# Optimization experiments

Hardware: AMD Instinct MI355X
Metric: run time of the kernel (lower is better)

## Reference

```python
import jax, jax.numpy as jnp
import numpy as np

FEATURE_DIM = 256
NUM_COEDGES = 200000


def setup_inputs() -> dict:
    key = jax.random.key(0)
    ks = jax.random.split(key, 13)
    d = FEATURE_DIM
    n = NUM_COEDGES
    scale = 1.0 / np.sqrt(d)
    inp = {
        "features": jax.random.normal(ks[0], (n, d), dtype=jnp.float32),
        "next_indices": jax.random.randint(ks[1], (n,), 0, n),
        "prev_indices": jax.random.randint(ks[2], (n,), 0, n),
        "mate_indices": jax.random.randint(ks[3], (n,), 0, n),
        # Linear params (torch Linear: y = x @ W.T + b); store as [d, d] for x @ W
        "W_self": jax.random.uniform(ks[4], (d, d), jnp.float32, -scale, scale),
        "b_self": jax.random.uniform(ks[5], (d,), jnp.float32, -scale, scale),
        "W_next": jax.random.uniform(ks[6], (d, d), jnp.float32, -scale, scale),
        "b_next": jax.random.uniform(ks[7], (d,), jnp.float32, -scale, scale),
        "W_prev": jax.random.uniform(ks[8], (d, d), jnp.float32, -scale, scale),
        "b_prev": jax.random.uniform(ks[9], (d,), jnp.float32, -scale, scale),
        "W_mate": jax.random.uniform(ks[10], (d, d), jnp.float32, -scale, scale),
        "b_mate": jax.random.uniform(ks[11], (d,), jnp.float32, -scale, scale),
    }
    return inp


def reference(features, next_indices, prev_indices, mate_indices,
              W_self, b_self, W_next, b_next, W_prev, b_prev, W_mate, b_mate):
    h = features  # [n, d]
    h_self = h @ W_self + b_self
    h_next = h[next_indices] @ W_next + b_next
    h_prev = h[prev_indices] @ W_prev + b_prev
    h_mate = h[mate_indices] @ W_mate + b_mate
    return jax.nn.relu(h_self + h_next + h_prev + h_mate)
```

## Files before the change

### kernel.cpp

```cpp
#include <hip/hip_runtime.h>
#include <stdint.h>


#define D 256
#define BM 64

typedef __bf16 bf16x8 __attribute__((ext_vector_type(8)));
typedef float f32x4 __attribute__((ext_vector_type(4)));

static __device__ __forceinline__ uint16_t f32_to_bf16_rne(uint32_t u) {
    return (uint16_t)((u + 0x7FFFu + ((u >> 16) & 1u)) >> 16);
}

__global__ void k_conv(const float* __restrict__ f, uint16_t* __restrict__ o, long total) {
    long base = (long)blockIdx.x * 2048;
    int t = threadIdx.x;
#pragma unroll
    for (int pass = 0; pass < 2; pass++) {
        long i = base + pass * 1024 + (long)t * 4;
        if (i + 4 > total) return;
        uint32_t v[4];
        *(uint4*)v = *(const uint4*)(f + i);
        union { uint16_t u16[4]; uint2 v2; } r;
#pragma unroll
        for (int j = 0; j < 4; j++) r.u16[j] = f32_to_bf16_rne(v[j]);
        *(uint2*)(o + i) = r.v2;
    }
}

__global__ void k_pack(const float* __restrict__ Ws, const float* __restrict__ Wn,
                       const float* __restrict__ Wp, const float* __restrict__ Wm,
                       uint16_t* __restrict__ Bp) {
    int b = blockIdx.x;
    int l = threadIdx.x;
    int ksg = b >> 4, nt = b & 15;
    int ph = ksg >> 3;
    const float* W = (ph == 0) ? Ws : (ph == 1) ? Wn : (ph == 2) ? Wp : Wm;
    int kl = (ksg & 7) * 32 + (l >> 4) * 8;
    int n  = nt * 16 + (l & 15);
    uint16_t* dst = Bp + ((size_t)b * 64 + l) * 8;
#pragma unroll
    for (int j = 0; j < 8; j++) {
        uint32_t u = __builtin_bit_cast(uint32_t, W[(size_t)(kl + j) * D + n]);
        dst[j] = f32_to_bf16_rne(u);
    }
}

__global__ void k_bias(const float* __restrict__ b0, const float* __restrict__ b1,
                       const float* __restrict__ b2, const float* __restrict__ b3,
                       float* __restrict__ btot) {
    int t = threadIdx.x;
    if (t < D) btot[t] = b0[t] + b1[t] + b2[t] + b3[t];
}

typedef __attribute__((address_space(1))) uint32_t gu32;
typedef __attribute__((address_space(3))) uint32_t lu32;

__global__ __launch_bounds__(256, 2) void k_gemm(
    const uint16_t* __restrict__ fb,
    const int* __restrict__ ni, const int* __restrict__ pi, const int* __restrict__ mi,
    const uint16_t* __restrict__ Bp, const float* __restrict__ btot,
    float* __restrict__ out, int nrows)
{
    __shared__ uint16_t As[2][BM * D];
    const int t  = threadIdx.x;
    const int w  = t >> 6;
    const int l  = t & 63;
    const int ml = l & 15;
    const int q  = l >> 4;
    const int m0 = blockIdx.x * BM;

    f32x4 acc[4][4] = {};

    const int rpar = w * 16 + (l >> 5);
    const int cs   = l & 31;

    uint32_t off0[8], off1[8], off2[8], off3[8];
#pragma unroll
    for (int e = 0; e < 8; e++) {
        int r = rpar + e * 2;
        int rowg = m0 + r; if (rowg >= nrows) rowg = nrows - 1;
        uint32_t co = (uint32_t)((cs ^ (r & 7)) * 16);
        off0[e] = (uint32_t)rowg * (D * 2) + co;
        off1[e] = (uint32_t)ni[rowg] * (D * 2) + co;
        off2[e] = (uint32_t)pi[rowg] * (D * 2) + co;
        off3[e] = (uint32_t)mi[rowg] * (D * 2) + co;
    }

#define STAGE(OFFA, BUF) do { \
        uint16_t* _s = &As[BUF][(w * 16) * D]; \
        _Pragma("unroll") \
        for (int e = 0; e < 8; e++) { \
            const char* _g = (const char*)fb + (OFFA)[e]; \
            __builtin_amdgcn_global_load_lds((const gu32*)_g, (lu32*)(_s + e * 2 * D), 16, 0, 0); \
        } \
    } while (0)

#define KSTEP(BUF, BB, KS) do { \
        bf16x8 bfr[4]; \
        _Pragma("unroll") \
        for (int j = 0; j < 4; j++) bfr[j] = *(const bf16x8*)((BB) + ((KS) * 16 + j) * 512); \
        bf16x8 afr[4]; \
        _Pragma("unroll") \
        for (int mt = 0; mt < 4; mt++) { \
            int r = mt * 16 + ml; \
            int ch = ((KS) * 4 + q) ^ (r & 7); \
            afr[mt] = *(const bf16x8*)&As[BUF][r * D + ch * 8]; \
        } \
        _Pragma("unroll") \
        for (int mt = 0; mt < 4; mt++) \
            _Pragma("unroll") \
            for (int j = 0; j < 4; j++) \
                acc[mt][j] = __builtin_amdgcn_mfma_f32_16x16x32_bf16(afr[mt], bfr[j], acc[mt][j], 0, 0, 0); \
    } while (0)

#define KSTEP_PRE(BUF, BPRE, KS) do { \
        bf16x8 afr[4]; \
        _Pragma("unroll") \
        for (int mt = 0; mt < 4; mt++) { \
            int r = mt * 16 + ml; \
            int ch = ((KS) * 4 + q) ^ (r & 7); \
            afr[mt] = *(const bf16x8*)&As[BUF][r * D + ch * 8]; \
        } \
        _Pragma("unroll") \
        for (int mt = 0; mt < 4; mt++) \
            _Pragma("unroll") \
            for (int j = 0; j < 4; j++) \
                acc[mt][j] = __builtin_amdgcn_mfma_f32_16x16x32_bf16(afr[mt], (BPRE)[j], acc[mt][j], 0, 0, 0); \
    } while (0)

#define WAITBAR() do { \
        asm volatile("s_waitcnt vmcnt(0)" ::: "memory"); \
        __builtin_amdgcn_s_barrier(); \
        __builtin_amdgcn_sched_barrier(0); \
    } while (0)

#define PHASE(P, BUF, OFFNEXT, LAST) do { \
        WAITBAR(); \
        const uint16_t* bb = Bp + (((size_t)(P) * 128 + w * 4) * 64 + l) * 8; \
        KSTEP(BUF, bb, 0); KSTEP(BUF, bb, 1); KSTEP(BUF, bb, 2); \
        KSTEP(BUF, bb, 3); KSTEP(BUF, bb, 4); KSTEP(BUF, bb, 5); \
        bf16x8 b6[4], b7[4]; \
        _Pragma("unroll") \
        for (int j = 0; j < 4; j++) { \
            b6[j] = *(const bf16x8*)(bb + (6 * 16 + j) * 512); \
            b7[j] = *(const bf16x8*)(bb + (7 * 16 + j) * 512); \
        } \
        if (!(LAST)) { \
            __builtin_amdgcn_sched_barrier(0); \
            STAGE(OFFNEXT, (BUF) ^ 1); \
            __builtin_amdgcn_sched_barrier(0); \
        } \
        KSTEP_PRE(BUF, b6, 6); \
        KSTEP_PRE(BUF, b7, 7); \
    } while (0)

    STAGE(off0, 0);
    PHASE(0, 0, off1, 0);
    PHASE(1, 1, off2, 0);
    PHASE(2, 0, off3, 0);
    PHASE(3, 1, off0, 1);

#undef PHASE
#undef WAITBAR
#undef KSTEP_PRE
#undef KSTEP
#undef STAGE

#pragma unroll
    for (int j = 0; j < 4; j++) {
        int n = (w * 4 + j) * 16 + ml;
        float bv = btot[n];
#pragma unroll
        for (int mt = 0; mt < 4; mt++) {
#pragma unroll
            for (int rg = 0; rg < 4; rg++) {
                int row = m0 + mt * 16 + q * 4 + rg;
                if (row < nrows) {
                    float v = acc[mt][j][rg] + bv;
                    out[(size_t)row * D + n] = v > 0.f ? v : 0.f;
                }
            }
        }
    }
}

__global__ void k_naive(const float* __restrict__ f,
                        const int* __restrict__ ni, const int* __restrict__ pi,
                        const int* __restrict__ mi,
                        const float* __restrict__ Ws, const float* __restrict__ bs,
                        const float* __restrict__ Wn, const float* __restrict__ bn,
                        const float* __restrict__ Wp, const float* __restrict__ bp,
                        const float* __restrict__ Wm, const float* __restrict__ bm,
                        float* __restrict__ out) {
    int row = blockIdx.x, n = threadIdx.x;
    const float* f0 = f + (size_t)row * D;
    const float* f1 = f + (size_t)ni[row] * D;
    const float* f2 = f + (size_t)pi[row] * D;
    const float* f3 = f + (size_t)mi[row] * D;
    float s = bs[n] + bn[n] + bp[n] + bm[n];
    for (int k = 0; k < D; k++)
        s += f0[k] * Ws[k * D + n] + f1[k] * Wn[k * D + n] +
             f2[k] * Wp[k * D + n] + f3[k] * Wm[k * D + n];
    out[(size_t)row * D + n] = s > 0.f ? s : 0.f;
}

extern "C" void kernel_launch(void* const* d_in, const int* in_sizes, int n_in,
                              void* d_out, int out_size, void* d_ws, size_t ws_size,
                              hipStream_t stream) {
    const float* feat = (const float*)d_in[0];
    const int*   ni   = (const int*)d_in[1];
    const int*   pi   = (const int*)d_in[2];
    const int*   mi   = (const int*)d_in[3];
    const float* Ws   = (const float*)d_in[4];
    const float* bs   = (const float*)d_in[5];
    const float* Wn   = (const float*)d_in[6];
    const float* bn   = (const float*)d_in[7];
    const float* Wp   = (const float*)d_in[8];
    const float* bp   = (const float*)d_in[9];
    const float* Wm   = (const float*)d_in[10];
    const float* bm   = (const float*)d_in[11];
    float* out = (float*)d_out;

    int nrows = in_sizes[1];
    size_t feat_elems = (size_t)nrows * D;
    size_t fb_bytes   = feat_elems * 2;
    size_t bp_off     = fb_bytes;
    size_t bias_off   = bp_off + (size_t)1024 * D * 2;
    size_t need       = bias_off + (size_t)D * 4;

    if (ws_size < need) {
        k_naive<<<nrows, D, 0, stream>>>(feat, ni, pi, mi, Ws, bs, Wn, bn, Wp, bp, Wm, bm, out);
        return;
    }

    uint16_t* fbuf = (uint16_t*)d_ws;
    uint16_t* Bpk  = (uint16_t*)((char*)d_ws + bp_off);
    float*    btot = (float*)((char*)d_ws + bias_off);

    long total = (long)feat_elems;
    int cblocks = (int)((total + 2047) / 2048);
    k_conv<<<cblocks, 256, 0, stream>>>(feat, fbuf, total);
    k_pack<<<512, 64, 0, stream>>>(Ws, Wn, Wp, Wm, Bpk);
    k_bias<<<1, 256, 0, stream>>>(bs, bn, bp, bm, btot);
    k_gemm<<<(nrows + BM - 1) / BM, 256, 0, stream>>>(fbuf, ni, pi, mi, Bpk, btot, out, nrows);
}
```

Baseline: 537.6 us.

## Use 128-row tiles with 8 waves and register-staged single LDS buffer

The GEMM tile grows from 64 to 128 rows with 512 threads arranged as 2x4 waves, so each packed weight fragment loaded from global memory is reused across twice as many rows. The double-buffered LDS with async global_load_lds is replaced by register staging: the next phase's gathered rows go into registers during compute and are written to a single LDS buffer after a barrier. The bias-sum kernel is folded into the weight-pack kernel as an extra block, removing one launch. In exchange there is extra register pressure and a second barrier per phase, and the LDS write is no longer overlapped with compute.

After: 575.0 us. 7.0% more time.

```diff
diff --git a/kernel.cpp b/kernel.cpp
--- a/kernel.cpp
+++ b/kernel.cpp
@@ -3,7 +3,7 @@
 
 
 #define D 256
-#define BM 64
+#define BM 128
 
 typedef __bf16 bf16x8 __attribute__((ext_vector_type(8)));
 typedef float f32x4 __attribute__((ext_vector_type(4)));
@@ -30,9 +30,19 @@
 
 __global__ void k_pack(const float* __restrict__ Ws, const float* __restrict__ Wn,
                        const float* __restrict__ Wp, const float* __restrict__ Wm,
-                       uint16_t* __restrict__ Bp) {
+                       const float* __restrict__ bs, const float* __restrict__ bn,
+                       const float* __restrict__ bp, const float* __restrict__ bm,
+                       uint16_t* __restrict__ Bp, float* __restrict__ btot) {
     int b = blockIdx.x;
     int l = threadIdx.x;
+    if (b == 512) {
+#pragma unroll
+        for (int k = 0; k < 4; k++) {
+            int n = l + k * 64;
+            btot[n] = bs[n] + bn[n] + bp[n] + bm[n];
+        }
+        return;
+    }
     int ksg = b >> 4, nt = b & 15;
     int ph = ksg >> 3;
     const float* W = (ph == 0) ? Ws : (ph == 1) ? Wn : (ph == 2) ? Wp : Wm;
@@ -46,28 +56,20 @@
     }
 }
 
-__global__ void k_bias(const float* __restrict__ b0, const float* __restrict__ b1,
-                       const float* __restrict__ b2, const float* __restrict__ b3,
-                       float* __restrict__ btot) {
-    int t = threadIdx.x;
-    if (t < D) btot[t] = b0[t] + b1[t] + b2[t] + b3[t];
-}
-
-typedef __attribute__((address_space(1))) uint32_t gu32;
-typedef __attribute__((address_space(3))) uint32_t lu32;
-
-__global__ __launch_bounds__(256, 2) void k_gemm(
+__global__ __launch_bounds__(512, 2) void k_gemm(
     const uint16_t* __restrict__ fb,
     const int* __restrict__ ni, const int* __restrict__ pi, const int* __restrict__ mi,
     const uint16_t* __restrict__ Bp, const float* __restrict__ btot,
     float* __restrict__ out, int nrows)
 {
-    __shared__ uint16_t As[2][BM * D];
+    __shared__ uint16_t As[BM * D];
     const int t  = threadIdx.x;
     const int w  = t >> 6;
     const int l  = t & 63;
     const int ml = l & 15;
     const int q  = l >> 4;
+    const int wr = w >> 2;
+    const int wc = w & 3;
     const int m0 = blockIdx.x * BM;
 
     f32x4 acc[4][4] = {};
@@ -75,107 +77,99 @@
     const int rpar = w * 16 + (l >> 5);
     const int cs   = l & 31;
 
-    uint32_t off0[8], off1[8], off2[8], off3[8];
+    uint32_t off0[8], off1[8], off2[8], off3[8], loff[8];
 #pragma unroll
     for (int e = 0; e < 8; e++) {
         int r = rpar + e * 2;
         int rowg = m0 + r; if (rowg >= nrows) rowg = nrows - 1;
-        uint32_t co = (uint32_t)((cs ^ (r & 7)) * 16);
+        uint32_t co = (uint32_t)(cs * 16);
         off0[e] = (uint32_t)rowg * (D * 2) + co;
         off1[e] = (uint32_t)ni[rowg] * (D * 2) + co;
         off2[e] = (uint32_t)pi[rowg] * (D * 2) + co;
         off3[e] = (uint32_t)mi[rowg] * (D * 2) + co;
-    }
-
-#define STAGE(OFFA, BUF) do { \
-        uint16_t* _s = &As[BUF][(w * 16) * D]; \
-        _Pragma("unroll") \
-        for (int e = 0; e < 8; e++) { \
-            const char* _g = (const char*)fb + (OFFA)[e]; \
-            __builtin_amdgcn_global_load_lds((const gu32*)_g, (lu32*)(_s + e * 2 * D), 16, 0, 0); \
-        } \
-    } while (0)
-
-#define KSTEP(BUF, BB, KS) do { \
-        bf16x8 bfr[4]; \
-        _Pragma("unroll") \
-        for (int j = 0; j < 4; j++) bfr[j] = *(const bf16x8*)((BB) + ((KS) * 16 + j) * 512); \
-        bf16x8 afr[4]; \
+        loff[e] = (uint32_t)r * (D * 2) + (uint32_t)((cs ^ (r & 7)) * 16);
+    }
+
+    uint4 st[8];
+
+#define STAGE_LOAD(OFFA) do { \
+        _Pragma("unroll") \
+        for (int e = 0; e < 8; e++) \
+            st[e] = *(const uint4*)((const char*)fb + (OFFA)[e]); \
+    } while (0)
+
+#define STAGE_WRITE() do { \
+        _Pragma("unroll") \
+        for (int e = 0; e < 8; e++) \
+            *(uint4*)((char*)As + loff[e]) = st[e]; \
+    } while (0)
+
+#define LOADB(DST, KS) do { \
+        _Pragma("unroll") \
+        for (int j = 0; j < 4; j++) \
+            (DST)[j] = *(const bf16x8*)(bb + ((KS) * 16 + j) * 512); \
+    } while (0)
+
+#define MM(BREG, KS) do { \
         _Pragma("unroll") \
         for (int mt = 0; mt < 4; mt++) { \
-            int r = mt * 16 + ml; \
-            int ch = ((KS) * 4 + q) ^ (r & 7); \
-            afr[mt] = *(const bf16x8*)&As[BUF][r * D + ch * 8]; \
-        } \
-        _Pragma("unroll") \
-        for (int mt = 0; mt < 4; mt++) \
+            int r  = wr * 64 + mt * 16 + ml; \
+            int ch = ((KS) * 4 + q) ^ (r & 7);             \
+            bf16x8 afr = *(const bf16x8*)&As[r * D + ch * 8]; \
             _Pragma("unroll") \
             for (int j = 0; j < 4; j++) \
-                acc[mt][j] = __builtin_amdgcn_mfma_f32_16x16x32_bf16(afr[mt], bfr[j], acc[mt][j], 0, 0, 0); \
-    } while (0)
-
-#define KSTEP_PRE(BUF, BPRE, KS) do { \
-        bf16x8 afr[4]; \
-        _Pragma("unroll") \
-        for (int mt = 0; mt < 4; mt++) { \
-            int r = mt * 16 + ml; \
-            int ch = ((KS) * 4 + q) ^ (r & 7); \
-            afr[mt] = *(const bf16x8*)&As[BUF][r * D + ch * 8]; \
+                acc[mt][j] = __builtin_amdgcn_mfma_f32_16x16x32_bf16( \
+                    afr, (BREG)[j], acc[mt][j], 0, 0, 0); \
         } \
-        _Pragma("unroll") \
-        for (int mt = 0; mt < 4; mt++) \
-            _Pragma("unroll") \
-            for (int j = 0; j < 4; j++) \
-                acc[mt][j] = __builtin_amdgcn_mfma_f32_16x16x32_bf16(afr[mt], (BPRE)[j], acc[mt][j], 0, 0, 0); \
-    } while (0)
-
-#define WAITBAR() do { \
-        asm volatile("s_waitcnt vmcnt(0)" ::: "memory"); \
+    } while (0)
+
+#define PHASE(P, OFFNEXT, LAST) do { \
         __builtin_amdgcn_s_barrier(); \
         __builtin_amdgcn_sched_barrier(0); \
-    } while (0)
-
-#define PHASE(P, BUF, OFFNEXT, LAST) do { \
-        WAITBAR(); \
-        const uint16_t* bb = Bp + (((size_t)(P) * 128 + w * 4) * 64 + l) * 8; \
-        KSTEP(BUF, bb, 0); KSTEP(BUF, bb, 1); KSTEP(BUF, bb, 2); \
-        KSTEP(BUF, bb, 3); KSTEP(BUF, bb, 4); KSTEP(BUF, bb, 5); \
-        bf16x8 b6[4], b7[4]; \
-        _Pragma("unroll") \
-        for (int j = 0; j < 4; j++) { \
-            b6[j] = *(const bf16x8*)(bb + (6 * 16 + j) * 512); \
-            b7[j] = *(const bf16x8*)(bb + (7 * 16 + j) * 512); \
-        } \
+        STAGE_WRITE(); \
+        asm volatile("s_waitcnt lgkmcnt(0)" ::: "memory"); \
+        __builtin_amdgcn_s_barrier(); \
+        __builtin_amdgcn_sched_barrier(0); \
+        const uint16_t* bb = Bp + (((size_t)(P) * 128 + wc * 4) * 64 + l) * 8; \
+        bf16x8 Ba[4], Bb[4]; \
+        LOADB(Ba, 0); \
+        LOADB(Bb, 1); MM(Ba, 0); \
+        LOADB(Ba, 2); MM(Bb, 1); \
+        LOADB(Bb, 3); MM(Ba, 2); \
+        LOADB(Ba, 4); MM(Bb, 3); \
+        LOADB(Bb, 5); MM(Ba, 4); \
+        LOADB(Ba, 6); MM(Bb, 5); \
+        LOADB(Bb, 7); \
         if (!(LAST)) { \
             __builtin_amdgcn_sched_barrier(0); \
-            STAGE(OFFNEXT, (BUF) ^ 1); \
+            STAGE_LOAD(OFFNEXT); \
             __builtin_amdgcn_sched_barrier(0); \
         } \
-        KSTEP_PRE(BUF, b6, 6); \
-        KSTEP_PRE(BUF, b7, 7); \
-    } while (0)
-
-    STAGE(off0, 0);
-    PHASE(0, 0, off1, 0);
-    PHASE(1, 1, off2, 0);
-    PHASE(2, 0, off3, 0);
-    PHASE(3, 1, off0, 1);
+        MM(Ba, 6); \
+        MM(Bb, 7); \
+    } while (0)
+
+    STAGE_LOAD(off0);
+    PHASE(0, off1, 0);
+    PHASE(1, off2, 0);
+    PHASE(2, off3, 0);
+    PHASE(3, off0, 1);
 
 #undef PHASE
-#undef WAITBAR
-#undef KSTEP_PRE
-#undef KSTEP
-#undef STAGE
+#undef MM
+#undef LOADB
+#undef STAGE_WRITE
+#undef STAGE_LOAD
 
 #pragma unroll
     for (int j = 0; j < 4; j++) {
-        int n = (w * 4 + j) * 16 + ml;
+        int n = (wc * 4 + j) * 16 + ml;
         float bv = btot[n];
 #pragma unroll
         for (int mt = 0; mt < 4; mt++) {
 #pragma unroll
             for (int rg = 0; rg < 4; rg++) {
-                int row = m0 + mt * 16 + q * 4 + rg;
+                int row = m0 + wr * 64 + mt * 16 + q * 4 + rg;
                 if (row < nrows) {
                     float v = acc[mt][j][rg] + bv;
                     out[(size_t)row * D + n] = v > 0.f ? v : 0.f;
@@ -241,7 +235,6 @@
     long total = (long)feat_elems;
     int cblocks = (int)((total + 2047) / 2048);
     k_conv<<<cblocks, 256, 0, stream>>>(feat, fbuf, total);
-    k_pack<<<512, 64, 0, stream>>>(Ws, Wn, Wp, Wm, Bpk);
-    k_bias<<<1, 256, 0, stream>>>(bs, bn, bp, bm, btot);
-    k_gemm<<<(nrows + BM - 1) / BM, 256, 0, stream>>>(fbuf, ni, pi, mi, Bpk, btot, out, nrows);
-}
+    k_pack<<<513, 64, 0, stream>>>(Ws, Wn, Wp, Wm, bs, bn, bp, bm, Bpk, btot);
+    k_gemm<<<(nrows + BM - 1) / BM, 512, 0, stream>>>(fbuf, ni, pi, mi, Bpk, btot, out, nrows);
+}
```
